# Optimization experiments

Measured on AMD Instinct MI355X. Metric: run time of the kernel, lower is better.

The kernel has to match this reference:

```python
import jax, jax.numpy as jnp
import numpy as np

N, E = 500000, 128
H1, H2, H3, OUT = 256, 128, 64, 1
IN = 3 * E


def setup_inputs() -> dict:
    key = jax.random.key(0)
    ks = jax.random.split(key, 12)
    s = 0.02
    return {
        "encoder": jax.random.normal(ks[0], (N, E), dtype=jnp.float32),
        "current_state_tsr": jax.random.randint(ks[1], (N, 1), 0, 2, dtype=jnp.int32),
        "W1": jax.random.normal(ks[2], (IN, H1), dtype=jnp.float32) * s,
        "b1": jnp.zeros((H1,), dtype=jnp.float32),
        "W2": jax.random.normal(ks[3], (H1, H2), dtype=jnp.float32) * s,
        "b2": jnp.zeros((H2,), dtype=jnp.float32),
        "W3": jax.random.normal(ks[4], (H2, H3), dtype=jnp.float32) * s,
        "b3": jnp.zeros((H3,), dtype=jnp.float32),
        "W4": jax.random.normal(ks[5], (H3, OUT), dtype=jnp.float32) * s,
        "b4": jnp.zeros((OUT,), dtype=jnp.float32),
        "graph": 1,
    }


def reference(encoder, current_state_tsr, W1, b1, W2, b2, W3, b3, W4, b4, graph):
    n = encoder.shape[0]
    cs = current_state_tsr  # [N,1] int state flags
    # masked node features (zeros where mask fails), then single-graph max readout
    in_state = jnp.where(cs > 0, encoder, 0.0)            # [N,E]
    mu_in = jax.nn.relu(jnp.max(in_state, axis=0, keepdims=True))   # [1,E]
    not_in_state = jnp.where(cs == 0, encoder, 0.0)       # [N,E]
    mu_not = jax.nn.relu(jnp.max(not_in_state, axis=0, keepdims=True))  # [1,E]
    feats = jnp.concatenate(
        [jnp.broadcast_to(mu_in, (n, mu_in.shape[1])),
         jnp.broadcast_to(mu_not, (n, mu_not.shape[1])),
         encoder], axis=1)                                # [N,3E]
    h = jax.nn.leaky_relu(feats @ W1 + b1)
    h = jax.nn.leaky_relu(h @ W2 + b2)
    h = jax.nn.leaky_relu(h @ W3 + b3)
    logits = h @ W4 + b4                                  # [N,1]
    q = jax.nn.softmax(logits, axis=0)                    # softmax across nodes
    return q.squeeze(axis=1)                              # [N]
```

## Files before the change

kernel.cpp:

```cpp
#include <hip/hip_runtime.h>
#include <hip/hip_bf16.h>

#define NN 500000
#define NBLK_CM 2000

typedef unsigned short ushort_t;
typedef __attribute__((ext_vector_type(8))) __bf16 bf16x8;
typedef __attribute__((ext_vector_type(2))) __bf16 bf16x2;
typedef __attribute__((ext_vector_type(4))) float f32x4;
typedef __attribute__((ext_vector_type(4))) unsigned uint4v;

__device__ inline ushort_t f2bf(float f) {
  unsigned u = __builtin_bit_cast(unsigned, f);
  return (ushort_t)((u + 0x7FFFu + ((u >> 16) & 1u)) >> 16);
}
__device__ inline float lrelu(float v) { return fmaxf(v, 0.f) + 0.01f * fminf(v, 0.f); }
__device__ inline unsigned pk2(float lo, float hi) {
  bf16x2 v; v[0] = (__bf16)lo; v[1] = (__bf16)hi;
  return __builtin_bit_cast(unsigned, v);
}
__device__ inline bf16x8 mk8(unsigned w0, unsigned w1, unsigned w2, unsigned w3) {
  uint4v u; u.x = w0; u.y = w1; u.z = w2; u.w = w3;
  return __builtin_bit_cast(bf16x8, u);
}
#define SHF_X(v, m) ((unsigned)__shfl_xor((int)(v), (m), 64))
#define SBAR() __builtin_amdgcn_sched_barrier(0)

__device__ inline void bfly4(unsigned q0, unsigned q1, unsigned q2, unsigned q3,
                             bool b0, bool b1,
                             unsigned& w0, unsigned& w1, unsigned& w2, unsigned& w3)
{
  unsigned vA0 = b1 ? q0 : q2, vA1 = b1 ? q1 : q3;
  unsigned eA0 = SHF_X(vA0, 32), eA1 = SHF_X(vA1, 32);
  unsigned s00 = b1 ? eA0 : q0, s01 = b1 ? eA1 : q1;
  unsigned s10 = b1 ? q2 : eA0, s11 = b1 ? q3 : eA1;
  unsigned vB0 = b0 ? s00 : s10, vB1 = b0 ? s01 : s11;
  unsigned eB0 = SHF_X(vB0, 16), eB1 = SHF_X(vB1, 16);
  w0 = b0 ? eB0 : s00; w1 = b0 ? eB1 : s01;
  w2 = b0 ? s10 : eB0; w3 = b0 ? s11 : eB1;
}

__global__ __launch_bounds__(256) void k_colmax(
    const float* __restrict__ enc, const int* __restrict__ cs,
    float* __restrict__ partials)
{
  __shared__ float4 s_in[256], s_not[256];
  const int tid = threadIdx.x;
  const int c4 = tid & 31;
  const int rs = tid >> 5;
  const long base = (long)blockIdx.x * 250;
  float4 mi = {0.f, 0.f, 0.f, 0.f}, mn = {0.f, 0.f, 0.f, 0.f};
  const float4* e4 = (const float4*)enc;
  #pragma unroll 4
  for (int it = 0; it < 32; ++it) {
    long r = base + rs + 8L * it;
    if (r < base + 250 && r < NN) {
      float4 v = e4[r * 32 + c4];
      bool ins = cs[r] > 0;
      mi.x = fmaxf(mi.x, ins ? v.x : 0.f); mi.y = fmaxf(mi.y, ins ? v.y : 0.f);
      mi.z = fmaxf(mi.z, ins ? v.z : 0.f); mi.w = fmaxf(mi.w, ins ? v.w : 0.f);
      mn.x = fmaxf(mn.x, ins ? 0.f : v.x); mn.y = fmaxf(mn.y, ins ? 0.f : v.y);
      mn.z = fmaxf(mn.z, ins ? 0.f : v.z); mn.w = fmaxf(mn.w, ins ? 0.f : v.w);
    }
  }
  s_in[tid] = mi; s_not[tid] = mn;
  __syncthreads();
  if (tid < 32) {
    for (int j = 1; j < 8; ++j) {
      float4 a = s_in[j * 32 + tid], b = s_not[j * 32 + tid];
      mi.x = fmaxf(mi.x, a.x); mi.y = fmaxf(mi.y, a.y);
      mi.z = fmaxf(mi.z, a.z); mi.w = fmaxf(mi.w, a.w);
      mn.x = fmaxf(mn.x, b.x); mn.y = fmaxf(mn.y, b.y);
      mn.z = fmaxf(mn.z, b.z); mn.w = fmaxf(mn.w, b.w);
    }
    float* po = partials + (size_t)blockIdx.x * 256;
    ((float4*)po)[tid] = mi;
    ((float4*)(po + 128))[tid] = mn;
  }
}

__global__ __launch_bounds__(256) void k_red1(
    const float* __restrict__ partials, float* __restrict__ red2)
{
  const int tid = threadIdx.x, b = blockIdx.x;
  float m = 0.f;
  #pragma unroll 8
  for (int row = b; row < NBLK_CM; row += 64)
    m = fmaxf(m, partials[(size_t)row * 256 + tid]);
  red2[b * 256 + tid] = m;
}

__global__ __launch_bounds__(1024) void k_red2(
    const float* __restrict__ red2,
    float* __restrict__ mu_in, float* __restrict__ mu_not)
{
  __shared__ float sT[1024];
  const int tid = threadIdx.x;
  const int col = tid & 255, sl = tid >> 8;
  float m = 0.f;
  #pragma unroll
  for (int j = 0; j < 16; ++j)
    m = fmaxf(m, red2[(sl * 16 + j) * 256 + col]);
  sT[tid] = m;
  __syncthreads();
  if (tid < 256) {
    m = fmaxf(fmaxf(sT[tid], sT[tid + 256]), fmaxf(sT[tid + 512], sT[tid + 768]));
    if (tid < 128) mu_in[tid] = m;
    else           mu_not[tid - 128] = m;
  }
}

__global__ __launch_bounds__(512)
__attribute__((amdgpu_waves_per_eu(2, 2)))
void k_mlp(
    const float* __restrict__ enc,
    const float* __restrict__ W1, const float* __restrict__ b1,
    const float* __restrict__ W2, const float* __restrict__ b2,
    const float* __restrict__ W3, const float* __restrict__ b3,
    const float* __restrict__ W4, const float* __restrict__ b4,
    const float* __restrict__ mu_in, const float* __restrict__ mu_not,
    float* __restrict__ eL, float* __restrict__ psum)
{
  __shared__ ushort_t sW1[256 * 128];
  __shared__ ushort_t sW2[128 * 256];
  __shared__ ushort_t sW3[64 * 128];
  __shared__ float sC[520];
  __shared__ float sT[512];

  const int tid = threadIdx.x;

  for (int idx = tid; idx < 32768; idx += 512) {
    int n = idx & 255, k = idx >> 8;
    int bp = ((k >> 3) + 2 * n) & 15;
    sW1[n * 128 + bp * 8 + (k & 7)] = f2bf(W1[(256 + k) * 256 + n]);
  }
  for (int idx = tid; idx < 32768; idx += 512) {
    int n = idx & 127, k = idx >> 7;
    int bp = ((k >> 3) + 2 * n) & 31;
    sW2[n * 256 + bp * 8 + (k & 7)] = f2bf(W2[k * 128 + n]);
  }
  for (int idx = tid; idx < 8192; idx += 512) {
    int n = idx & 63, k = idx >> 6;
    int bp = ((k >> 3) + 2 * n) & 15;
    sW3[n * 128 + bp * 8 + (k & 7)] = f2bf(W3[k * 64 + n]);
  }
  if (tid >= 256 && tid < 384) sC[tid] = b2[tid - 256];
  else if (tid >= 384 && tid < 448) sC[tid] = b3[tid - 384];
  else if (tid >= 448) sC[tid] = W4[tid - 448];
  if (tid == 0) sC[512] = b4[0];
  {
    const int j = tid & 255, h = tid >> 8;
    float c = h ? 0.f : b1[j];
    #pragma unroll 8
    for (int e = 64 * h; e < 64 * h + 64; ++e) {
      c += mu_in[e]  * W1[e * 256 + j];
      c += mu_not[e] * W1[(128 + e) * 256 + j];
    }
    sT[tid] = c;
  }
  __syncthreads();
  if (tid < 256) sC[tid] = sT[tid] + sT[tid + 256];
  __syncthreads();

  const int wave = tid >> 6, lane = tid & 63;
  const int lr = lane & 15, lg = lane >> 4;
  const int wid = blockIdx.x * 8 + wave;
  const bool b0 = lg & 1, b1f = lg & 2;
  const int sw = lg + 2 * lr;

  const ushort_t* w1p = sW1 + lr * 128;
  const ushort_t* w2p = sW2 + lr * 256;
  const ushort_t* w3p = sW3 + lr * 128;

  float es = 0.f;
  bf16x8 B1[4];

  {
    const float4* p = (const float4*)(enc + (size_t)(wid * 16 + lr) * 128);
    #pragma unroll
    for (int kt = 0; kt < 4; ++kt) {
      float4 f0 = p[kt * 8 + lg * 2], f1 = p[kt * 8 + lg * 2 + 1];
      bf16x8 a;
      a[0] = (__bf16)f0.x; a[1] = (__bf16)f0.y; a[2] = (__bf16)f0.z; a[3] = (__bf16)f0.w;
      a[4] = (__bf16)f1.x; a[5] = (__bf16)f1.y; a[6] = (__bf16)f1.z; a[7] = (__bf16)f1.w;
      B1[kt] = a;
    }
  }

  for (int r0 = wid * 16; r0 < NN; r0 += 32768) {
    bf16x8 B2[8];
    #pragma unroll
    for (int p = 0; p < 8; ++p) {
      f32x4 a0 = (f32x4){0.f, 0.f, 0.f, 0.f}, a1 = (f32x4){0.f, 0.f, 0.f, 0.f};
      #pragma unroll
      for (int kt = 0; kt < 4; ++kt) {
        bf16x8 wA = *(const bf16x8*)(w1p + (2 * p) * 2048 + (((4 * kt + sw) & 15) << 3));
        bf16x8 wB = *(const bf16x8*)(w1p + (2 * p + 1) * 2048 + (((4 * kt + sw) & 15) << 3));
        a0 = __builtin_amdgcn_mfma_f32_16x16x32_bf16(wA, B1[kt], a0, 0, 0, 0);
        a1 = __builtin_amdgcn_mfma_f32_16x16x32_bf16(wB, B1[kt], a1, 0, 0, 0);
      }
      float4 cb0 = *(const float4*)(sC + 16 * (2 * p) + 4 * lg);
      float4 cb1 = *(const float4*)(sC + 16 * (2 * p + 1) + 4 * lg);
      unsigned q0 = pk2(lrelu(a0[0] + cb0.x), lrelu(a0[1] + cb0.y));
      unsigned q1 = pk2(lrelu(a0[2] + cb0.z), lrelu(a0[3] + cb0.w));
      unsigned q2 = pk2(lrelu(a1[0] + cb1.x), lrelu(a1[1] + cb1.y));
      unsigned q3 = pk2(lrelu(a1[2] + cb1.z), lrelu(a1[3] + cb1.w));
      unsigned w0, w1, w2, w3;
      bfly4(q0, q1, q2, q3, b0, b1f, w0, w1, w2, w3);
      B2[p] = mk8(w0, w1, w2, w3);
    }
    SBAR();
    bf16x8 B3[4];
    #pragma unroll
    for (int p = 0; p < 4; ++p) {
      f32x4 a0 = (f32x4){0.f, 0.f, 0.f, 0.f}, a1 = (f32x4){0.f, 0.f, 0.f, 0.f};
      #pragma unroll
      for (int kt = 0; kt < 8; ++kt) {
        bf16x8 wA = *(const bf16x8*)(w2p + (2 * p) * 4096 + (((4 * kt + sw) & 31) << 3));
        bf16x8 wB = *(const bf16x8*)(w2p + (2 * p + 1) * 4096 + (((4 * kt + sw) & 31) << 3));
        a0 = __builtin_amdgcn_mfma_f32_16x16x32_bf16(wA, B2[kt], a0, 0, 0, 0);
        a1 = __builtin_amdgcn_mfma_f32_16x16x32_bf16(wB, B2[kt], a1, 0, 0, 0);
      }
      float4 cb0 = *(const float4*)(sC + 256 + 16 * (2 * p) + 4 * lg);
      float4 cb1 = *(const float4*)(sC + 256 + 16 * (2 * p + 1) + 4 * lg);
      unsigned q0 = pk2(lrelu(a0[0] + cb0.x), lrelu(a0[1] + cb0.y));
      unsigned q1 = pk2(lrelu(a0[2] + cb0.z), lrelu(a0[3] + cb0.w));
      unsigned q2 = pk2(lrelu(a1[0] + cb1.x), lrelu(a1[1] + cb1.y));
      unsigned q3 = pk2(lrelu(a1[2] + cb1.z), lrelu(a1[3] + cb1.w));
      unsigned w0, w1, w2, w3;
      bfly4(q0, q1, q2, q3, b0, b1f, w0, w1, w2, w3);
      B3[p] = mk8(w0, w1, w2, w3);
    }
    SBAR();
    int rn = r0 + 32768; if (rn >= NN) rn = r0;
    float4 tA[8];
    {
      const float4* p = (const float4*)(enc + (size_t)(rn + lr) * 128);
      #pragma unroll
      for (int kt = 0; kt < 4; ++kt) {
        tA[2 * kt]     = p[kt * 8 + lg * 2];
        tA[2 * kt + 1] = p[kt * 8 + lg * 2 + 1];
      }
    }
    SBAR();
    float dot = 0.f;
    #pragma unroll
    for (int p = 0; p < 2; ++p) {
      f32x4 a0 = (f32x4){0.f, 0.f, 0.f, 0.f}, a1 = (f32x4){0.f, 0.f, 0.f, 0.f};
      #pragma unroll
      for (int kt = 0; kt < 4; ++kt) {
        bf16x8 wA = *(const bf16x8*)(w3p + (2 * p) * 2048 + (((4 * kt + sw) & 15) << 3));
        bf16x8 wB = *(const bf16x8*)(w3p + (2 * p + 1) * 2048 + (((4 * kt + sw) & 15) << 3));
        a0 = __builtin_amdgcn_mfma_f32_16x16x32_bf16(wA, B3[kt], a0, 0, 0, 0);
        a1 = __builtin_amdgcn_mfma_f32_16x16x32_bf16(wB, B3[kt], a1, 0, 0, 0);
      }
      float4 cb0  = *(const float4*)(sC + 384 + 16 * (2 * p) + 4 * lg);
      float4 cb1  = *(const float4*)(sC + 384 + 16 * (2 * p + 1) + 4 * lg);
      float4 w4v0 = *(const float4*)(sC + 448 + 16 * (2 * p) + 4 * lg);
      float4 w4v1 = *(const float4*)(sC + 448 + 16 * (2 * p + 1) + 4 * lg);
      dot += lrelu(a0[0] + cb0.x) * w4v0.x + lrelu(a0[1] + cb0.y) * w4v0.y
           + lrelu(a0[2] + cb0.z) * w4v0.z + lrelu(a0[3] + cb0.w) * w4v0.w;
      dot += lrelu(a1[0] + cb1.x) * w4v1.x + lrelu(a1[1] + cb1.y) * w4v1.y
           + lrelu(a1[2] + cb1.z) * w4v1.z + lrelu(a1[3] + cb1.w) * w4v1.w;
    }
    dot += __shfl_xor(dot, 16, 64);
    dot += __shfl_xor(dot, 32, 64);
    float ev = expf(dot + sC[512]);
    if (lg == 0) eL[r0 + lr] = ev;
    es += ev;
    #pragma unroll
    for (int kt = 0; kt < 4; ++kt) {
      float4 f0 = tA[2 * kt], f1 = tA[2 * kt + 1];
      bf16x8 a;
      a[0] = (__bf16)f0.x; a[1] = (__bf16)f0.y; a[2] = (__bf16)f0.z; a[3] = (__bf16)f0.w;
      a[4] = (__bf16)f1.x; a[5] = (__bf16)f1.y; a[6] = (__bf16)f1.z; a[7] = (__bf16)f1.w;
      B1[kt] = a;
    }
  }
  #pragma unroll
  for (int off = 1; off < 64; off <<= 1) es += __shfl_xor(es, off, 64);
  if (lane == 0) psum[wid] = 0.25f * es;
}

__global__ __launch_bounds__(256) void k_finalsum(const float* __restrict__ psum,
                                                  float* __restrict__ scal)
{
  const int tid = threadIdx.x;
  float s = 0.f;
  #pragma unroll
  for (int k = 0; k < 8; ++k) s += psum[tid + k * 256];
  #pragma unroll
  for (int off = 1; off < 64; off <<= 1) s += __shfl_xor(s, off, 64);
  __shared__ float sr[4];
  if ((tid & 63) == 0) sr[tid >> 6] = s;
  __syncthreads();
  if (tid == 0) scal[0] = 1.f / (sr[0] + sr[1] + sr[2] + sr[3]);
}

__global__ __launch_bounds__(256) void k_norm(const float* __restrict__ eL,
                                              const float* __restrict__ scal,
                                              float* __restrict__ out)
{
  const float inv = scal[0];
  const int i = blockIdx.x * 256 + threadIdx.x;
  if (i < NN / 4) {
    float4 v = ((const float4*)eL)[i];
    float4 o = {v.x * inv, v.y * inv, v.z * inv, v.w * inv};
    ((float4*)out)[i] = o;
  }
}

extern "C" void kernel_launch(void* const* d_in, const int* in_sizes, int n_in,
                              void* d_out, int out_size, void* d_ws, size_t ws_size,
                              hipStream_t stream) {
  const float* enc = (const float*)d_in[0];
  const int*   cs  = (const int*)d_in[1];
  const float* W1  = (const float*)d_in[2];
  const float* b1  = (const float*)d_in[3];
  const float* W2  = (const float*)d_in[4];
  const float* b2  = (const float*)d_in[5];
  const float* W3  = (const float*)d_in[6];
  const float* b3  = (const float*)d_in[7];
  const float* W4  = (const float*)d_in[8];
  const float* b4  = (const float*)d_in[9];
  float* out = (float*)d_out;

  char* ws = (char*)d_ws;
  float* mu_in  = (float*)(ws + 0);
  float* mu_not = (float*)(ws + 512);
  float* psum   = (float*)(ws + 2048);
  float* scal   = (float*)(ws + 10240);
  float* red2   = (float*)(ws + 16384);
  float* eLbuf  = (float*)(ws + 131072);
  float* partials = (float*)(ws + 131072);

  k_colmax<<<dim3(NBLK_CM), dim3(256), 0, stream>>>(enc, cs, partials);
  k_red1<<<dim3(64), dim3(256), 0, stream>>>(partials, red2);
  k_red2<<<dim3(1), dim3(1024), 0, stream>>>(red2, mu_in, mu_not);
  k_mlp<<<dim3(256), dim3(512), 0, stream>>>(enc, W1, b1, W2, b2, W3, b3, W4, b4,
                                             mu_in, mu_not, eLbuf, psum);
  k_finalsum<<<dim3(1), dim3(256), 0, stream>>>(psum, scal);
  k_norm<<<dim3(489), dim3(256), 0, stream>>>(eLbuf, scal, out);
}
```

Baseline: 182.9 us.

## Process two 16-row tiles per wave to reuse LDS weight fragments

Each wave now handles 32 rows per iteration as two independent 16-row tiles. Every weight fragment read from LDS feeds two MFMAs instead of one, roughly halving LDS weight traffic per row across all three layers. The grid stride doubles, and the next tile's encoder prefetch now covers both halves. The cost is about twice the live VGPRs for activations, accumulators and prefetch buffers, which may lower occupancy or cause spills.

```diff
diff --git a/kernel.cpp b/kernel.cpp
--- a/kernel.cpp
+++ b/kernel.cpp
@@ -173,108 +173,153 @@
   const ushort_t* w3p = sW3 + lr * 128;
 
   float es = 0.f;
-  bf16x8 B1[4];
+  bf16x8 B1a[4], B1b[4];
 
   {
-    const float4* p = (const float4*)(enc + (size_t)(wid * 16 + lr) * 128);
+    const float4* pa = (const float4*)(enc + (size_t)(wid * 32 + lr) * 128);
+    const float4* pb = (const float4*)(enc + (size_t)(wid * 32 + 16 + lr) * 128);
     #pragma unroll
     for (int kt = 0; kt < 4; ++kt) {
-      float4 f0 = p[kt * 8 + lg * 2], f1 = p[kt * 8 + lg * 2 + 1];
-      bf16x8 a;
+      float4 f0 = pa[kt * 8 + lg * 2], f1 = pa[kt * 8 + lg * 2 + 1];
+      float4 g0 = pb[kt * 8 + lg * 2], g1 = pb[kt * 8 + lg * 2 + 1];
+      bf16x8 a, b;
       a[0] = (__bf16)f0.x; a[1] = (__bf16)f0.y; a[2] = (__bf16)f0.z; a[3] = (__bf16)f0.w;
       a[4] = (__bf16)f1.x; a[5] = (__bf16)f1.y; a[6] = (__bf16)f1.z; a[7] = (__bf16)f1.w;
-      B1[kt] = a;
-    }
-  }
-
-  for (int r0 = wid * 16; r0 < NN; r0 += 32768) {
-    bf16x8 B2[8];
+      b[0] = (__bf16)g0.x; b[1] = (__bf16)g0.y; b[2] = (__bf16)g0.z; b[3] = (__bf16)g0.w;
+      b[4] = (__bf16)g1.x; b[5] = (__bf16)g1.y; b[6] = (__bf16)g1.z; b[7] = (__bf16)g1.w;
+      B1a[kt] = a; B1b[kt] = b;
+    }
+  }
+
+  for (int r0 = wid * 32; r0 < NN; r0 += 65536) {
+    bf16x8 B2a[8], B2b[8];
     #pragma unroll
     for (int p = 0; p < 8; ++p) {
-      f32x4 a0 = (f32x4){0.f, 0.f, 0.f, 0.f}, a1 = (f32x4){0.f, 0.f, 0.f, 0.f};
+      f32x4 aA0 = (f32x4){0.f,0.f,0.f,0.f}, aA1 = (f32x4){0.f,0.f,0.f,0.f};
+      f32x4 aB0 = (f32x4){0.f,0.f,0.f,0.f}, aB1 = (f32x4){0.f,0.f,0.f,0.f};
       #pragma unroll
       for (int kt = 0; kt < 4; ++kt) {
         bf16x8 wA = *(const bf16x8*)(w1p + (2 * p) * 2048 + (((4 * kt + sw) & 15) << 3));
         bf16x8 wB = *(const bf16x8*)(w1p + (2 * p + 1) * 2048 + (((4 * kt + sw) & 15) << 3));
-        a0 = __builtin_amdgcn_mfma_f32_16x16x32_bf16(wA, B1[kt], a0, 0, 0, 0);
-        a1 = __builtin_amdgcn_mfma_f32_16x16x32_bf16(wB, B1[kt], a1, 0, 0, 0);
+        aA0 = __builtin_amdgcn_mfma_f32_16x16x32_bf16(wA, B1a[kt], aA0, 0, 0, 0);
+        aA1 = __builtin_amdgcn_mfma_f32_16x16x32_bf16(wB, B1a[kt], aA1, 0, 0, 0);
+        aB0 = __builtin_amdgcn_mfma_f32_16x16x32_bf16(wA, B1b[kt], aB0, 0, 0, 0);
+        aB1 = __builtin_amdgcn_mfma_f32_16x16x32_bf16(wB, B1b[kt], aB1, 0, 0, 0);
       }
       float4 cb0 = *(const float4*)(sC + 16 * (2 * p) + 4 * lg);
       float4 cb1 = *(const float4*)(sC + 16 * (2 * p + 1) + 4 * lg);
-      unsigned q0 = pk2(lrelu(a0[0] + cb0.x), lrelu(a0[1] + cb0.y));
-      unsigned q1 = pk2(lrelu(a0[2] + cb0.z), lrelu(a0[3] + cb0.w));
-      unsigned q2 = pk2(lrelu(a1[0] + cb1.x), lrelu(a1[1] + cb1.y));
-      unsigned q3 = pk2(lrelu(a1[2] + cb1.z), lrelu(a1[3] + cb1.w));
-      unsigned w0, w1, w2, w3;
-      bfly4(q0, q1, q2, q3, b0, b1f, w0, w1, w2, w3);
-      B2[p] = mk8(w0, w1, w2, w3);
+      {
+        unsigned q0 = pk2(lrelu(aA0[0] + cb0.x), lrelu(aA0[1] + cb0.y));
+        unsigned q1 = pk2(lrelu(aA0[2] + cb0.z), lrelu(aA0[3] + cb0.w));
+        unsigned q2 = pk2(lrelu(aA1[0] + cb1.x), lrelu(aA1[1] + cb1.y));
+        unsigned q3 = pk2(lrelu(aA1[2] + cb1.z), lrelu(aA1[3] + cb1.w));
+        unsigned w0, w1, w2, w3;
+        bfly4(q0, q1, q2, q3, b0, b1f, w0, w1, w2, w3);
+        B2a[p] = mk8(w0, w1, w2, w3);
+      }
+      {
+        unsigned q0 = pk2(lrelu(aB0[0] + cb0.x), lrelu(aB0[1] + cb0.y));
+        unsigned q1 = pk2(lrelu(aB0[2] + cb0.z), lrelu(aB0[3] + cb0.w));
+        unsigned q2 = pk2(lrelu(aB1[0] + cb1.x), lrelu(aB1[1] + cb1.y));
+        unsigned q3 = pk2(lrelu(aB1[2] + cb1.z), lrelu(aB1[3] + cb1.w));
+        unsigned w0, w1, w2, w3;
+        bfly4(q0, q1, q2, q3, b0, b1f, w0, w1, w2, w3);
+        B2b[p] = mk8(w0, w1, w2, w3);
+      }
     }
     SBAR();
-    bf16x8 B3[4];
+    bf16x8 B3a[4], B3b[4];
     #pragma unroll
     for (int p = 0; p < 4; ++p) {
-      f32x4 a0 = (f32x4){0.f, 0.f, 0.f, 0.f}, a1 = (f32x4){0.f, 0.f, 0.f, 0.f};
+      f32x4 aA0 = (f32x4){0.f,0.f,0.f,0.f}, aA1 = (f32x4){0.f,0.f,0.f,0.f};
+      f32x4 aB0 = (f32x4){0.f,0.f,0.f,0.f}, aB1 = (f32x4){0.f,0.f,0.f,0.f};
       #pragma unroll
       for (int kt = 0; kt < 8; ++kt) {
         bf16x8 wA = *(const bf16x8*)(w2p + (2 * p) * 4096 + (((4 * kt + sw) & 31) << 3));
         bf16x8 wB = *(const bf16x8*)(w2p + (2 * p + 1) * 4096 + (((4 * kt + sw) & 31) << 3));
-        a0 = __builtin_amdgcn_mfma_f32_16x16x32_bf16(wA, B2[kt], a0, 0, 0, 0);
-        a1 = __builtin_amdgcn_mfma_f32_16x16x32_bf16(wB, B2[kt], a1, 0, 0, 0);
+        aA0 = __builtin_amdgcn_mfma_f32_16x16x32_bf16(wA, B2a[kt], aA0, 0, 0, 0);
+        aA1 = __builtin_amdgcn_mfma_f32_16x16x32_bf16(wB, B2a[kt], aA1, 0, 0, 0);
+        aB0 = __builtin_amdgcn_mfma_f32_16x16x32_bf16(wA, B2b[kt], aB0, 0, 0, 0);
+        aB1 = __builtin_amdgcn_mfma_f32_16x16x32_bf16(wB, B2b[kt], aB1, 0, 0, 0);
       }
       float4 cb0 = *(const float4*)(sC + 256 + 16 * (2 * p) + 4 * lg);
       float4 cb1 = *(const float4*)(sC + 256 + 16 * (2 * p + 1) + 4 * lg);
-      unsigned q0 = pk2(lrelu(a0[0] + cb0.x), lrelu(a0[1] + cb0.y));
-      unsigned q1 = pk2(lrelu(a0[2] + cb0.z), lrelu(a0[3] + cb0.w));
-      unsigned q2 = pk2(lrelu(a1[0] + cb1.x), lrelu(a1[1] + cb1.y));
-      unsigned q3 = pk2(lrelu(a1[2] + cb1.z), lrelu(a1[3] + cb1.w));
-      unsigned w0, w1, w2, w3;
-      bfly4(q0, q1, q2, q3, b0, b1f, w0, w1, w2, w3);
-      B3[p] = mk8(w0, w1, w2, w3);
+      {
+        unsigned q0 = pk2(lrelu(aA0[0] + cb0.x), lrelu(aA0[1] + cb0.y));
+        unsigned q1 = pk2(lrelu(aA0[2] + cb0.z), lrelu(aA0[3] + cb0.w));
+        unsigned q2 = pk2(lrelu(aA1[0] + cb1.x), lrelu(aA1[1] + cb1.y));
+        unsigned q3 = pk2(lrelu(aA1[2] + cb1.z), lrelu(aA1[3] + cb1.w));
+        unsigned w0, w1, w2, w3;
+        bfly4(q0, q1, q2, q3, b0, b1f, w0, w1, w2, w3);
+        B3a[p] = mk8(w0, w1, w2, w3);
+      }
+      {
+        unsigned q0 = pk2(lrelu(aB0[0] + cb0.x), lrelu(aB0[1] + cb0.y));
+        unsigned q1 = pk2(lrelu(aB0[2] + cb0.z), lrelu(aB0[3] + cb0.w));
+        unsigned q2 = pk2(lrelu(aB1[0] + cb1.x), lrelu(aB1[1] + cb1.y));
+        unsigned q3 = pk2(lrelu(aB1[2] + cb1.z), lrelu(aB1[3] + cb1.w));
+        unsigned w0, w1, w2, w3;
+        bfly4(q0, q1, q2, q3, b0, b1f, w0, w1, w2, w3);
+        B3b[p] = mk8(w0, w1, w2, w3);
+      }
     }
     SBAR();
-    int rn = r0 + 32768; if (rn >= NN) rn = r0;
-    float4 tA[8];
+    int rn = r0 + 65536; if (rn >= NN) rn = r0;
+    float4 tA[8], tB[8];
     {
-      const float4* p = (const float4*)(enc + (size_t)(rn + lr) * 128);
+      const float4* pa = (const float4*)(enc + (size_t)(rn + lr) * 128);
+      const float4* pb = (const float4*)(enc + (size_t)(rn + 16 + lr) * 128);
       #pragma unroll
       for (int kt = 0; kt < 4; ++kt) {
-        tA[2 * kt]     = p[kt * 8 + lg * 2];
-        tA[2 * kt + 1] = p[kt * 8 + lg * 2 + 1];
+        tA[2 * kt]     = pa[kt * 8 + lg * 2];
+        tA[2 * kt + 1] = pa[kt * 8 + lg * 2 + 1];
+        tB[2 * kt]     = pb[kt * 8 + lg * 2];
+        tB[2 * kt + 1] = pb[kt * 8 + lg * 2 + 1];
       }
     }
     SBAR();
-    float dot = 0.f;
+    float da = 0.f, db = 0.f;
     #pragma unroll
     for (int p = 0; p < 2; ++p) {
-      f32x4 a0 = (f32x4){0.f, 0.f, 0.f, 0.f}, a1 = (f32x4){0.f, 0.f, 0.f, 0.f};
+      f32x4 aA0 = (f32x4){0.f,0.f,0.f,0.f}, aA1 = (f32x4){0.f,0.f,0.f,0.f};
+      f32x4 aB0 = (f32x4){0.f,0.f,0.f,0.f}, aB1 = (f32x4){0.f,0.f,0.f,0.f};
       #pragma unroll
       for (int kt = 0; kt < 4; ++kt) {
         bf16x8 wA = *(const bf16x8*)(w3p + (2 * p) * 2048 + (((4 * kt + sw) & 15) << 3));
         bf16x8 wB = *(const bf16x8*)(w3p + (2 * p + 1) * 2048 + (((4 * kt + sw) & 15) << 3));
-        a0 = __builtin_amdgcn_mfma_f32_16x16x32_bf16(wA, B3[kt], a0, 0, 0, 0);
-        a1 = __builtin_amdgcn_mfma_f32_16x16x32_bf16(wB, B3[kt], a1, 0, 0, 0);
+        aA0 = __builtin_amdgcn_mfma_f32_16x16x32_bf16(wA, B3a[kt], aA0, 0, 0, 0);
+        aA1 = __builtin_amdgcn_mfma_f32_16x16x32_bf16(wB, B3a[kt], aA1, 0, 0, 0);
+        aB0 = __builtin_amdgcn_mfma_f32_16x16x32_bf16(wA, B3b[kt], aB0, 0, 0, 0);
+        aB1 = __builtin_amdgcn_mfma_f32_16x16x32_bf16(wB, B3b[kt], aB1, 0, 0, 0);
       }
       float4 cb0  = *(const float4*)(sC + 384 + 16 * (2 * p) + 4 * lg);
       float4 cb1  = *(const float4*)(sC + 384 + 16 * (2 * p + 1) + 4 * lg);
       float4 w4v0 = *(const float4*)(sC + 448 + 16 * (2 * p) + 4 * lg);
       float4 w4v1 = *(const float4*)(sC + 448 + 16 * (2 * p + 1) + 4 * lg);
-      dot += lrelu(a0[0] + cb0.x) * w4v0.x + lrelu(a0[1] + cb0.y) * w4v0.y
-           + lrelu(a0[2] + cb0.z) * w4v0.z + lrelu(a0[3] + cb0.w) * w4v0.w;
-      dot += lrelu(a1[0] + cb1.x) * w4v1.x + lrelu(a1[1] + cb1.y) * w4v1.y
-           + lrelu(a1[2] + cb1.z) * w4v1.z + lrelu(a1[3] + cb1.w) * w4v1.w;
-    }
-    dot += __shfl_xor(dot, 16, 64);
-    dot += __shfl_xor(dot, 32, 64);
-    float ev = expf(dot + sC[512]);
-    if (lg == 0) eL[r0 + lr] = ev;
-    es += ev;
+      da += lrelu(aA0[0] + cb0.x) * w4v0.x + lrelu(aA0[1] + cb0.y) * w4v0.y
+          + lrelu(aA0[2] + cb0.z) * w4v0.z + lrelu(aA0[3] + cb0.w) * w4v0.w;
+      da += lrelu(aA1[0] + cb1.x) * w4v1.x + lrelu(aA1[1] + cb1.y) * w4v1.y
+          + lrelu(aA1[2] + cb1.z) * w4v1.z + lrelu(aA1[3] + cb1.w) * w4v1.w;
+      db += lrelu(aB0[0] + cb0.x) * w4v0.x + lrelu(aB0[1] + cb0.y) * w4v0.y
+          + lrelu(aB0[2] + cb0.z) * w4v0.z + lrelu(aB0[3] + cb0.w) * w4v0.w;
+      db += lrelu(aB1[0] + cb1.x) * w4v1.x + lrelu(aB1[1] + cb1.y) * w4v1.y
+          + lrelu(aB1[2] + cb1.z) * w4v1.z + lrelu(aB1[3] + cb1.w) * w4v1.w;
+    }
+    da += __shfl_xor(da, 16, 64); da += __shfl_xor(da, 32, 64);
+    db += __shfl_xor(db, 16, 64); db += __shfl_xor(db, 32, 64);
+    float eva = expf(da + sC[512]), evb = expf(db + sC[512]);
+    if (lg == 0) { eL[r0 + lr] = eva; eL[r0 + 16 + lr] = evb; }
+    es += eva + evb;
     #pragma unroll
     for (int kt = 0; kt < 4; ++kt) {
       float4 f0 = tA[2 * kt], f1 = tA[2 * kt + 1];
-      bf16x8 a;
+      float4 g0 = tB[2 * kt], g1 = tB[2 * kt + 1];
+      bf16x8 a, b;
       a[0] = (__bf16)f0.x; a[1] = (__bf16)f0.y; a[2] = (__bf16)f0.z; a[3] = (__bf16)f0.w;
       a[4] = (__bf16)f1.x; a[5] = (__bf16)f1.y; a[6] = (__bf16)f1.z; a[7] = (__bf16)f1.w;
-      B1[kt] = a;
+      b[0] = (__bf16)g0.x; b[1] = (__bf16)g0.y; b[2] = (__bf16)g0.z; b[3] = (__bf16)g0.w;
+      b[4] = (__bf16)g1.x; b[5] = (__bf16)g1.y; b[6] = (__bf16)g1.z; b[7] = (__bf16)g1.w;
+      B1a[kt] = a; B1b[kt] = b;
     }
   }
   #pragma unroll
```

After: 171.8 us. 6.1% less time.
